# Kernel tuning notes

Measured on AMD Instinct MI355X. Metric: run time of the kernel, lower is better.

The kernel has to match this reference:

```python
import jax, jax.numpy as jnp
import numpy as np

STATE_DIM = 2
HIDDEN = 1024
N_SKILLS = 5
N_ACTIONS = 4
BATCH = 65536


def setup_inputs() -> dict:
    key = jax.random.key(0)
    ks = jax.random.split(key, 8)
    def lin_init(k, fan_in, shape):
        bound = 1.0 / np.sqrt(fan_in)
        return jax.random.uniform(k, shape, jnp.float32, -bound, bound)
    return {
        "s": jax.random.normal(ks[0], (BATCH, STATE_DIM), jnp.float32),
        "skill_idx": jax.random.randint(ks[1], (BATCH,), 0, N_SKILLS, jnp.int32),
        "W1": lin_init(ks[2], STATE_DIM, (STATE_DIM, HIDDEN)),
        "b1": lin_init(ks[3], STATE_DIM, (HIDDEN,)),
        "W2": lin_init(ks[4], HIDDEN, (HIDDEN, HIDDEN)),
        "b2": lin_init(ks[5], HIDDEN, (HIDDEN,)),
        "W_heads": lin_init(ks[6], HIDDEN, (N_SKILLS, HIDDEN, N_ACTIONS)),
        "b_heads": lin_init(ks[7], HIDDEN, (N_SKILLS, N_ACTIONS)),
    }


def reference(s, skill_idx, W1, b1, W2, b2, W_heads, b_heads):
    # shared feature MLP: Linear -> ReLU -> Linear -> ReLU
    h = jax.nn.relu(s @ W1 + b1)            # [B, H]
    feat = jax.nn.relu(h @ W2 + b2)         # [B, H]
    # per-sample skill head: gather weights then one batched contraction
    Wg = W_heads[skill_idx]                 # [B, H, A]
    bg = b_heads[skill_idx]                 # [B, A]
    return jnp.einsum('bh,bha->ba', feat, Wg) + bg  # [B, A]
```

## Files before the change

### kernel.cpp

```cpp
#include <hip/hip_runtime.h>

typedef __bf16 bf16x8 __attribute__((ext_vector_type(8)));
typedef __bf16 bf16x4 __attribute__((ext_vector_type(4)));
typedef float  floatx4 __attribute__((ext_vector_type(4)));

#define GLOBAL_AS __attribute__((address_space(1)))
#define LOCAL_AS  __attribute__((address_space(3)))

static constexpr int HID = 1024;
static constexpr int BK  = 64;
static constexpr int KIT = HID / BK;

__device__ __forceinline__ void h8(bf16x8& d, float s0, float s1,
                                   const float4& w0a, const float4& w0b,
                                   const float4& w1a, const float4& w1b,
                                   const float4& ba,  const float4& bb) {
    d[0] = (__bf16)fmaxf(fmaf(s1, w1a.x, fmaf(s0, w0a.x, ba.x)), 0.f);
    d[1] = (__bf16)fmaxf(fmaf(s1, w1a.y, fmaf(s0, w0a.y, ba.y)), 0.f);
    d[2] = (__bf16)fmaxf(fmaf(s1, w1a.z, fmaf(s0, w0a.z, ba.z)), 0.f);
    d[3] = (__bf16)fmaxf(fmaf(s1, w1a.w, fmaf(s0, w0a.w, ba.w)), 0.f);
    d[4] = (__bf16)fmaxf(fmaf(s1, w1b.x, fmaf(s0, w0b.x, bb.x)), 0.f);
    d[5] = (__bf16)fmaxf(fmaf(s1, w1b.y, fmaf(s0, w0b.y, bb.y)), 0.f);
    d[6] = (__bf16)fmaxf(fmaf(s1, w1b.z, fmaf(s0, w0b.z, bb.z)), 0.f);
    d[7] = (__bf16)fmaxf(fmaf(s1, w1b.w, fmaf(s0, w0b.w, bb.w)), 0.f);
}

__global__ __launch_bounds__(256)
void prep_all(const float* __restrict__ W2, const float* __restrict__ WH,
              __bf16* __restrict__ W2T, __bf16* __restrict__ WHT,
              float* __restrict__ OUT) {
    int b = blockIdx.x;
    if (b < 256) {
        ((float4*)OUT)[(size_t)b * 256 + threadIdx.x]
            = make_float4(0.f, 0.f, 0.f, 0.f);
        return;
    }
    b -= 256;
    if (b < 256) {
        __shared__ __align__(16) __bf16 tile[64][72];
        const int bx = b & 15;
        const int by = b >> 4;
        const int a  = threadIdx.x & 63;
        const int bb = threadIdx.x >> 6;
#pragma unroll
        for (int r = 0; r < 16; ++r) {
            const int k = r * 4 + bb;
            tile[a][k] = (__bf16)W2[(size_t)(by * 64 + k) * HID + bx * 64 + a];
        }
        __syncthreads();
        const int slab = bx >> 2;
#pragma unroll
        for (int p = 0; p < 2; ++p) {
            const int idx = p * 256 + threadIdx.x;
            const int c   = idx & 63;
            const int oct = idx >> 6;
            const bf16x8 v = *(const bf16x8*)&tile[c][oct * 8];
            const int col = (bx & 3) * 64 + c;
            const size_t dst = ((size_t)(slab * KIT + by) * 8 + oct) * 256 + col;
            *(bf16x8*)(W2T + dst * 8) = v;
        }
    } else {
        const int r = b - 256;
        const int s = r >> 2, a = r & 3;
        for (int k = threadIdx.x; k < HID; k += 256) {
            const float v = (r < 20) ? WH[((size_t)s * HID + k) * 4 + a] : 0.f;
            WHT[(size_t)(k >> 3) * 256 + r * 8 + (k & 7)] = (__bf16)v;
        }
    }
}

__global__ __launch_bounds__(256, 3)
void policy_main(const float* __restrict__ S,  const int* __restrict__ SK,
                 const float* __restrict__ W1, const float* __restrict__ B1,
                 const __bf16* __restrict__ W2T, const float* __restrict__ B2,
                 const __bf16* __restrict__ WHT, const float* __restrict__ BH,
                 float* __restrict__ OUT) {
    __shared__ __align__(16) char smem[40960];
    __bf16* At    = (__bf16*)smem;
    __bf16* Bt    = (__bf16*)(smem + 8192);
    __bf16* featL = (__bf16*)(smem + 8192);

    const int tid  = threadIdx.x;
    const int lane = tid & 63;
    const int wv   = tid >> 6;
    const int l15  = lane & 15;
    const int quad = lane >> 4;
    const int slab = blockIdx.x >> 10;
    const int g    = blockIdx.x & 1023;
    const size_t i0 = (size_t)g * 64;

    const int octA = wv * 2 + (lane >> 5);
    const int smpA = lane & 31;

    floatx4 acc[4][4] = {};

    const float2 sv0 = *(const float2*)(S + (i0 + smpA) * 2);
    const float2 sv1 = *(const float2*)(S + (i0 + 32 + smpA) * 2);

#pragma unroll 1
    for (int kt = 0; kt < KIT; ++kt) {
        __syncthreads();
        const float* wp = W1 + kt * BK + octA * 8;
        const float4 w0a = *(const float4*)(wp);
        const float4 w0b = *(const float4*)(wp + 4);
        const float4 w1a = *(const float4*)(wp + HID);
        const float4 w1b = *(const float4*)(wp + HID + 4);
        const float4 ba  = *(const float4*)(B1 + kt * BK + octA * 8);
        const float4 bb  = *(const float4*)(B1 + kt * BK + octA * 8 + 4);
#pragma unroll
        for (int L = 0; L < 8; ++L) {
            const __bf16* gp = W2T
                + (((size_t)(slab * KIT + kt) * 8 + L) * 256 + wv * 64 + lane) * 8;
            __builtin_amdgcn_global_load_lds((GLOBAL_AS void*)gp,
                (LOCAL_AS void*)(Bt + (L * 256 + wv * 64) * 8), 16, 0, 0);
        }
        {
            bf16x8 hv;
            h8(hv, sv0.x, sv0.y, w0a, w0b, w1a, w1b, ba, bb);
            *(bf16x8*)(At + (octA * 64 + smpA) * 8) = hv;
            h8(hv, sv1.x, sv1.y, w0a, w0b, w1a, w1b, ba, bb);
            *(bf16x8*)(At + (octA * 64 + 32 + smpA) * 8) = hv;
        }
        __syncthreads();
#pragma unroll
        for (int ks = 0; ks < 2; ++ks) {
            bf16x8 wf[4], hf[4];
#pragma unroll
            for (int f = 0; f < 4; ++f)
                wf[f] = *(const bf16x8*)(Bt
                         + (((ks * 4 + quad) * 256) + wv * 64 + f * 16 + l15) * 8);
#pragma unroll
            for (int f = 0; f < 4; ++f)
                hf[f] = *(const bf16x8*)(At
                         + (((ks * 4 + quad) * 64) + f * 16 + l15) * 8);
#pragma unroll
            for (int fn = 0; fn < 4; ++fn)
#pragma unroll
                for (int fm = 0; fm < 4; ++fm)
                    acc[fn][fm] = __builtin_amdgcn_mfma_f32_16x16x32_bf16(
                        wf[fn], hf[fm], acc[fn][fm], 0, 0, 0);
        }
    }

    __syncthreads();
#pragma unroll
    for (int fn = 0; fn < 4; ++fn) {
        const int fcb = wv * 64 + fn * 16 + quad * 4;
        const float4 b2v = *(const float4*)(B2 + slab * 256 + fcb);
        const int o = fcb >> 3, j = fcb & 7;
#pragma unroll
        for (int fm = 0; fm < 4; ++fm) {
            const int smp = fm * 16 + l15;
            const floatx4 v = acc[fn][fm];
            bf16x4 p;
            p[0] = (__bf16)fmaxf(v[0] + b2v.x, 0.f);
            p[1] = (__bf16)fmaxf(v[1] + b2v.y, 0.f);
            p[2] = (__bf16)fmaxf(v[2] + b2v.z, 0.f);
            p[3] = (__bf16)fmaxf(v[3] + b2v.w, 0.f);
            *(bf16x4*)(featL + (o * 64 + smp) * 8 + j) = p;
        }
    }
    __syncthreads();

    floatx4 hacc[2] = {};
#pragma unroll
    for (int ks2 = 0; ks2 < 8; ++ks2) {
        const bf16x8 fa = *(const bf16x8*)(featL
                             + ((ks2 * 4 + quad) * 64 + wv * 16 + l15) * 8);
#pragma unroll
        for (int t2 = 0; t2 < 2; ++t2) {
            const int r  = t2 * 16 + l15;
            const int og = slab * 32 + ks2 * 4 + quad;
            const bf16x8 wb = *(const bf16x8*)(WHT + (size_t)og * 256 + r * 8);
            hacc[t2] = __builtin_amdgcn_mfma_f32_16x16x32_bf16(
                fa, wb, hacc[t2], 0, 0, 0);
        }
    }

#pragma unroll
    for (int j = 0; j < 4; ++j) {
        const int smp = wv * 16 + quad * 4 + j;
        const int sk  = SK[i0 + smp];
#pragma unroll
        for (int t2 = 0; t2 < 2; ++t2) {
            const int hc = t2 * 16 + l15;
            const int d  = hc - sk * 4;
            if (d >= 0 && d < 4) {
                float v = hacc[t2][j];
                if (slab == 0) v += BH[hc];
                atomicAdd(&OUT[(i0 + smp) * 4 + d], v);
            }
        }
    }
}

extern "C" void kernel_launch(void* const* d_in, const int* in_sizes, int n_in,
                              void* d_out, int out_size, void* d_ws, size_t ws_size,
                              hipStream_t stream) {
    const float* S  = (const float*)d_in[0];
    const int*   SK = (const int*)d_in[1];
    const float* W1 = (const float*)d_in[2];
    const float* B1 = (const float*)d_in[3];
    const float* W2 = (const float*)d_in[4];
    const float* B2 = (const float*)d_in[5];
    const float* WH = (const float*)d_in[6];
    const float* BH = (const float*)d_in[7];

    char* ws = (char*)d_ws;
    __bf16* W2T = (__bf16*)ws;
    __bf16* WHT = (__bf16*)(ws + 2 * 1024 * 1024);

    hipLaunchKernelGGL(prep_all, dim3(544), dim3(256), 0, stream,
                       W2, WH, W2T, WHT, (float*)d_out);
    hipLaunchKernelGGL(policy_main, dim3(4096), dim3(256), 0, stream,
                       S, SK, W1, B1, W2T, B2, WHT, BH, (float*)d_out);
}
```

Measured before the change: 220.9 us.

## Load W2 fragments directly from global and double-buffer the hidden tile

Drops the LDS staging of W2T through global_load_lds. Each wave now reads its W2 MFMA fragments straight from global memory into registers. The first-layer activation tile is double-buffered in LDS, with the next k-tile computed during the current MFMA step, so each iteration needs one barrier instead of two. This cuts LDS traffic and synchronisation but gives up shared reuse of W2 in LDS, relying on cache and per-lane global loads with possibly exposed latency.

Measured after the change: 220.2 us (median of 2 runs). Within noise of the previous version (-0.3%).

```diff
diff --git a/kernel.cpp b/kernel.cpp
--- a/kernel.cpp
+++ b/kernel.cpp
@@ -75,10 +75,9 @@
                  const __bf16* __restrict__ W2T, const float* __restrict__ B2,
                  const __bf16* __restrict__ WHT, const float* __restrict__ BH,
                  float* __restrict__ OUT) {
-    __shared__ __align__(16) char smem[40960];
+    __shared__ __align__(16) char smem[32768];
     __bf16* At    = (__bf16*)smem;
-    __bf16* Bt    = (__bf16*)(smem + 8192);
-    __bf16* featL = (__bf16*)(smem + 8192);
+    __bf16* featL = (__bf16*)smem;
 
     const int tid  = threadIdx.x;
     const int lane = tid & 63;
@@ -97,52 +96,82 @@
     const float2 sv0 = *(const float2*)(S + (i0 + smpA) * 2);
     const float2 sv1 = *(const float2*)(S + (i0 + 32 + smpA) * 2);
 
-#pragma unroll 1
-    for (int kt = 0; kt < KIT; ++kt) {
-        __syncthreads();
-        const float* wp = W1 + kt * BK + octA * 8;
+    {
+        const float* wp = W1 + octA * 8;
         const float4 w0a = *(const float4*)(wp);
         const float4 w0b = *(const float4*)(wp + 4);
         const float4 w1a = *(const float4*)(wp + HID);
         const float4 w1b = *(const float4*)(wp + HID + 4);
-        const float4 ba  = *(const float4*)(B1 + kt * BK + octA * 8);
-        const float4 bb  = *(const float4*)(B1 + kt * BK + octA * 8 + 4);
-#pragma unroll
-        for (int L = 0; L < 8; ++L) {
-            const __bf16* gp = W2T
-                + (((size_t)(slab * KIT + kt) * 8 + L) * 256 + wv * 64 + lane) * 8;
-            __builtin_amdgcn_global_load_lds((GLOBAL_AS void*)gp,
-                (LOCAL_AS void*)(Bt + (L * 256 + wv * 64) * 8), 16, 0, 0);
-        }
-        {
+        const float4 ba  = *(const float4*)(B1 + octA * 8);
+        const float4 bb  = *(const float4*)(B1 + octA * 8 + 4);
+        bf16x8 hv;
+        h8(hv, sv0.x, sv0.y, w0a, w0b, w1a, w1b, ba, bb);
+        *(bf16x8*)(At + (octA * 64 + smpA) * 8) = hv;
+        h8(hv, sv1.x, sv1.y, w0a, w0b, w1a, w1b, ba, bb);
+        *(bf16x8*)(At + (octA * 64 + 32 + smpA) * 8) = hv;
+    }
+    __syncthreads();
+
+    const __bf16* wbase = W2T + ((size_t)(slab * KIT) * 8 + quad) * 2048
+                        + (wv * 64 + l15) * 8;
+
+#pragma unroll 1
+    for (int kt = 0; kt < KIT; ++kt) {
+        const __bf16* Ac = At + (kt & 1) * 4096;
+        __bf16*       An = At + ((kt + 1) & 1) * 4096;
+
+        float4 w0a, w0b, w1a, w1b, ba, bb;
+        if (kt + 1 < KIT) {
+            const float* wp = W1 + (kt + 1) * BK + octA * 8;
+            w0a = *(const float4*)(wp);
+            w0b = *(const float4*)(wp + 4);
+            w1a = *(const float4*)(wp + HID);
+            w1b = *(const float4*)(wp + HID + 4);
+            ba  = *(const float4*)(B1 + (kt + 1) * BK + octA * 8);
+            bb  = *(const float4*)(B1 + (kt + 1) * BK + octA * 8 + 4);
+        }
+        bf16x8 wf0[4], wf1[4];
+        const __bf16* wkt = wbase + (size_t)kt * 8 * 2048;
+#pragma unroll
+        for (int f = 0; f < 4; ++f)
+            wf0[f] = *(const bf16x8*)(wkt + f * 16 * 8);
+#pragma unroll
+        for (int f = 0; f < 4; ++f)
+            wf1[f] = *(const bf16x8*)(wkt + 4 * 2048 + f * 16 * 8);
+        if (kt + 1 < KIT) {
             bf16x8 hv;
             h8(hv, sv0.x, sv0.y, w0a, w0b, w1a, w1b, ba, bb);
-            *(bf16x8*)(At + (octA * 64 + smpA) * 8) = hv;
+            *(bf16x8*)(An + (octA * 64 + smpA) * 8) = hv;
             h8(hv, sv1.x, sv1.y, w0a, w0b, w1a, w1b, ba, bb);
-            *(bf16x8*)(At + (octA * 64 + 32 + smpA) * 8) = hv;
-        }
-        __syncthreads();
-#pragma unroll
-        for (int ks = 0; ks < 2; ++ks) {
-            bf16x8 wf[4], hf[4];
+            *(bf16x8*)(An + (octA * 64 + 32 + smpA) * 8) = hv;
+        }
+        {
+            bf16x8 hf[4];
 #pragma unroll
             for (int f = 0; f < 4; ++f)
-                wf[f] = *(const bf16x8*)(Bt
-                         + (((ks * 4 + quad) * 256) + wv * 64 + f * 16 + l15) * 8);
-#pragma unroll
-            for (int f = 0; f < 4; ++f)
-                hf[f] = *(const bf16x8*)(At
-                         + (((ks * 4 + quad) * 64) + f * 16 + l15) * 8);
+                hf[f] = *(const bf16x8*)(Ac + ((quad * 64) + f * 16 + l15) * 8);
 #pragma unroll
             for (int fn = 0; fn < 4; ++fn)
 #pragma unroll
                 for (int fm = 0; fm < 4; ++fm)
                     acc[fn][fm] = __builtin_amdgcn_mfma_f32_16x16x32_bf16(
-                        wf[fn], hf[fm], acc[fn][fm], 0, 0, 0);
-        }
-    }
-
-    __syncthreads();
+                        wf0[fn], hf[fm], acc[fn][fm], 0, 0, 0);
+        }
+        {
+            bf16x8 hf[4];
+#pragma unroll
+            for (int f = 0; f < 4; ++f)
+                hf[f] = *(const bf16x8*)(Ac + (((4 + quad) * 64) + f * 16 + l15) * 8);
+#pragma unroll
+            for (int fn = 0; fn < 4; ++fn)
+#pragma unroll
+                for (int fm = 0; fm < 4; ++fm)
+                    acc[fn][fm] = __builtin_amdgcn_mfma_f32_16x16x32_bf16(
+                        wf1[fn], hf[fm], acc[fn][fm], 0, 0, 0);
+        }
+        __syncthreads();
+    }
+
 #pragma unroll
     for (int fn = 0; fn < 4; ++fn) {
         const int fcb = wv * 64 + fn * 16 + quad * 4;
```
